# Performance work log

Hardware: AMD Instinct MI355X
Metric: run time of the kernel (lower is better)

The kernel has to match this reference:

```python
import jax, jax.numpy as jnp
import numpy as np

E = 512      # embed_size
H = 8        # heads
HD = E // H  # head_dim
TN = 288     # time_num
FE = 4       # forward_expansion
N, T = 64, 512


def layernorm(x, g, b, eps=1e-5):
    mu = jnp.mean(x, axis=-1, keepdims=True)
    var = jnp.mean((x - mu) ** 2, axis=-1, keepdims=True)
    return (x - mu) * jax.lax.rsqrt(var + eps) * g + b


def setup_inputs() -> dict:
    key = jax.random.key(0)
    ks = jax.random.split(key, 12)
    w = lambda k, sh: jax.random.normal(k, sh, dtype=jnp.float32) * 0.02
    return {
        "value": jax.random.normal(ks[0], (N, T, E), dtype=jnp.float32),
        "key_in": jax.random.normal(ks[1], (N, T, E), dtype=jnp.float32),
        "query": jax.random.normal(ks[2], (N, T, E), dtype=jnp.float32),
        "i": 37,
        # One_hot_encoder params: learned identity-init table + linear to embed
        "I_mat": jnp.eye(TN, dtype=jnp.float32),
        "oh_W": w(ks[3], (TN, E)), "oh_b": jnp.zeros((E,), jnp.float32),
        # per-head projections (shared across heads, as in the torch module)
        "Wv": w(ks[4], (HD, HD)), "Wk": w(ks[5], (HD, HD)), "Wq": w(ks[6], (HD, HD)),
        "Wo": w(ks[7], (E, E)), "bo": jnp.zeros((E,), jnp.float32),
        "g1": jnp.ones((E,), jnp.float32), "b1": jnp.zeros((E,), jnp.float32),
        "g2": jnp.ones((E,), jnp.float32), "b2": jnp.zeros((E,), jnp.float32),
        "W1": w(ks[8], (E, FE * E)), "bf1": jnp.zeros((FE * E,), jnp.float32),
        "W2": w(ks[9], (FE * E, E)), "bf2": jnp.zeros((E,), jnp.float32),
    }


def reference(value, key_in, query, i, I_mat, oh_W, oh_b, Wv, Wk, Wq, Wo, bo,
              g1, b1, g2, b2, W1, bf1, W2, bf2):
    n, t, c = query.shape
    # One_hot_encoder: rows i..i+T-1 (mod time_num) of learned table -> linear
    rows = (i + jnp.arange(t)) % TN
    onehot = I_mat[rows] @ oh_W + oh_b            # (T, E), broadcast over N
    q_in = query + onehot[None, :, :]
    # per-head projections
    v = value.reshape(n, t, H, HD) @ Wv           # (N,T,H,HD)
    k = key_in.reshape(n, t, H, HD) @ Wk
    qh = q_in.reshape(n, t, H, HD) @ Wq
    # attention (note: scale uses sqrt(embed_size), per original code)
    energy = jnp.einsum("nqhd,nkhd->nhqk", qh, k) / jnp.sqrt(jnp.float32(E))
    attn = jax.nn.softmax(energy, axis=-1)
    out = jnp.einsum("nhqk,nkhd->nqhd", attn, v).reshape(n, t, E)
    out = out @ Wo + bo
    # residual + LN + FFN + residual + LN (dropout=0 -> identity)
    x = layernorm(out + q_in, g1, b1)
    ff = jax.nn.relu(x @ W1 + bf1) @ W2 + bf2
    return layernorm(ff + x, g2, b2)
```

## Files before the change

kernel.cpp:

```cpp
#include <hip/hip_runtime.h>

typedef __attribute__((ext_vector_type(8))) short s16x8;
typedef __attribute__((ext_vector_type(4))) float f32x4;

#define TN 288

__device__ __forceinline__ unsigned short f2bf(float f) {
  union { float f; unsigned u; } v; v.f = f;
  unsigned r = v.u + 0x7fffu + ((v.u >> 16) & 1u);
  return (unsigned short)(r >> 16);
}
__device__ __forceinline__ float bf2f(unsigned short u) {
  union { float f; unsigned u; } v; v.u = ((unsigned)u) << 16;
  return v.f;
}
__device__ __forceinline__ unsigned lds_addr(const void* p) {
  return (unsigned)(unsigned long long)(const __attribute__((address_space(3))) char*)p;
}
__device__ __forceinline__ void async_copy16(unsigned short* lds, const unsigned short* g) {
  __builtin_amdgcn_global_load_lds(
      (const __attribute__((address_space(1))) unsigned int*)g,
      (__attribute__((address_space(3))) unsigned int*)lds, 16, 0, 0);
}

__device__ __forceinline__ void pack_body(const float* __restrict__ W,
    unsigned short* __restrict__ out, int N, long t) {
  int lr = (int)(t & 15);
  int lg = (int)((t >> 4) & 3);
  long g6 = t >> 6;
  int nt = N >> 4;
  int n16 = (int)(g6 % nt);
  int kb = (int)(g6 / nt) << 5;
  int k = kb + lg * 8;
  int col = n16 * 16 + lr;
  s16x8 v;
#pragma unroll
  for (int j = 0; j < 8; ++j) v[j] = (short)f2bf(W[(size_t)(k + j) * N + col]);
  *(s16x8*)(out + t * 8) = v;
}

__global__ __launch_bounds__(256) void prep_kernel(const int* __restrict__ pi,
    const float* __restrict__ I_mat, const float* __restrict__ ohW,
    const float* __restrict__ ohb, float* __restrict__ onehot,
    const float* __restrict__ Wv, const float* __restrict__ Wk,
    const float* __restrict__ Wq, unsigned short* __restrict__ Wv_b,
    unsigned short* __restrict__ Wk_b, unsigned short* __restrict__ Wq_b,
    const float* __restrict__ Wo, const float* __restrict__ W1,
    const float* __restrict__ W2, unsigned short* __restrict__ Wop,
    unsigned short* __restrict__ W1p, unsigned short* __restrict__ W2p) {
  int b = blockIdx.x, tid = threadIdx.x;
  if (b < 512) {
    int t = b;
    int r = (pi[0] + t) % TN;
    float acc0 = ohb[tid], acc1 = ohb[tid + 256];
    const float* Ir = I_mat + (size_t)r * TN;
    for (int j = 0; j < TN; ++j) {
      float iv = Ir[j];
      acc0 += iv * ohW[(size_t)j * 512 + tid];
      acc1 += iv * ohW[(size_t)j * 512 + tid + 256];
    }
    onehot[(size_t)t * 512 + tid] = acc0;
    onehot[(size_t)t * 512 + tid + 256] = acc1;
  } else if (b < 640) {
    pack_body(Wo, Wop, 512, (long)(b - 512) * 256 + tid);
  } else if (b < 1152) {
    pack_body(W1, W1p, 2048, (long)(b - 640) * 256 + tid);
  } else if (b < 1664) {
    pack_body(W2, W2p, 512, (long)(b - 1152) * 256 + tid);
  } else {
    int which = b - 1664;
    const float* src = which == 0 ? Wv : (which == 1 ? Wk : Wq);
    unsigned short* dst = which == 0 ? Wv_b : (which == 1 ? Wk_b : Wq_b);
    float sc = which == 2 ? 0.06375871424f : 1.f;
#pragma unroll
    for (int j = 0; j < 4; ++j) {
      int i = tid * 16 + j * 4;
      float4 f = *(const float4*)(src + i);
      unsigned lo = (unsigned)f2bf(f.x * sc) | ((unsigned)f2bf(f.y * sc) << 16);
      unsigned hi = (unsigned)f2bf(f.z * sc) | ((unsigned)f2bf(f.w * sc) << 16);
      *(uint2*)(dst + i) = make_uint2(lo, hi);
    }
  }
}

__global__ __launch_bounds__(256) void proj_all(
    const float* __restrict__ value, const float* __restrict__ key_in,
    const float* __restrict__ query, const unsigned short* __restrict__ Wv_b,
    const unsigned short* __restrict__ Wk_b, const unsigned short* __restrict__ Wq_b,
    const float* __restrict__ onehot, unsigned short* __restrict__ vP,
    unsigned short* __restrict__ k_p, unsigned short* __restrict__ q_p) {
  __shared__ unsigned short As[64][40];
  __shared__ unsigned short Bs[64][40];
  __shared__ unsigned short Cs[64][72];
  const int which = blockIdx.x >> 12;
  const int mb = blockIdx.x & 4095;
  const float* A = which == 0 ? value : (which == 1 ? key_in : query);
  const unsigned short* B = which == 0 ? Wv_b : (which == 1 ? Wk_b : Wq_b);
  unsigned short* C = which == 0 ? vP : (which == 1 ? k_p : q_p);
  const bool qin = (which == 2);
  const int m0 = mb * 64;
  const int tid = threadIdx.x, w = tid >> 6, l = tid & 63, lr = l & 15, lg = l >> 4;
  const int wr = (w >> 1) * 32, wc = (w & 1) * 32;
  const int aRow = (tid * 8) >> 5, aK = (tid * 8) & 31;
  const int bK = (tid * 8) >> 6, bCol = (tid * 8) & 63;
  f32x4 acc[2][2] = {};
  for (int kb = 0; kb < 64; kb += 32) {
    size_t fl = (size_t)(m0 + aRow) * 64 + kb + aK;
    float4 f0 = *(const float4*)(A + fl);
    float4 f1 = *(const float4*)(A + fl + 4);
    if (qin) {
      const float* oh = onehot + (fl & 262143);
      float4 o0 = *(const float4*)(oh);
      float4 o1 = *(const float4*)(oh + 4);
      f0.x += o0.x; f0.y += o0.y; f0.z += o0.z; f0.w += o0.w;
      f1.x += o1.x; f1.y += o1.y; f1.z += o1.z; f1.w += o1.w;
    }
    s16x8 av;
    av[0] = (short)f2bf(f0.x); av[1] = (short)f2bf(f0.y);
    av[2] = (short)f2bf(f0.z); av[3] = (short)f2bf(f0.w);
    av[4] = (short)f2bf(f1.x); av[5] = (short)f2bf(f1.y);
    av[6] = (short)f2bf(f1.z); av[7] = (short)f2bf(f1.w);
    *(s16x8*)&As[aRow][aK] = av;
    s16x8 bv = *(const s16x8*)(B + (size_t)(kb + bK) * 64 + bCol);
#pragma unroll
    for (int j = 0; j < 8; ++j) Bs[bCol + j][bK] = (unsigned short)bv[j];
    __syncthreads();
    s16x8 af0 = *(const s16x8*)&As[wr + lr][lg * 8];
    s16x8 af1 = *(const s16x8*)&As[wr + 16 + lr][lg * 8];
    s16x8 bf0 = *(const s16x8*)&Bs[wc + lr][lg * 8];
    s16x8 bf1 = *(const s16x8*)&Bs[wc + 16 + lr][lg * 8];
    acc[0][0] = __builtin_amdgcn_mfma_f32_16x16x32_bf16(af0, bf0, acc[0][0], 0, 0, 0);
    acc[0][1] = __builtin_amdgcn_mfma_f32_16x16x32_bf16(af0, bf1, acc[0][1], 0, 0, 0);
    acc[1][0] = __builtin_amdgcn_mfma_f32_16x16x32_bf16(af1, bf0, acc[1][0], 0, 0, 0);
    acc[1][1] = __builtin_amdgcn_mfma_f32_16x16x32_bf16(af1, bf1, acc[1][1], 0, 0, 0);
    __syncthreads();
  }
  if (which != 0) {
#pragma unroll
    for (int fi = 0; fi < 2; ++fi)
#pragma unroll
      for (int fj = 0; fj < 2; ++fj)
#pragma unroll
        for (int r = 0; r < 4; ++r) {
          int row = m0 + wr + fi * 16 + lg * 4 + r;
          int col = wc + fj * 16 + lr;
          C[(size_t)row * 64 + col] = f2bf(acc[fi][fj][r]);
        }
  } else {
#pragma unroll
    for (int fi = 0; fi < 2; ++fi)
#pragma unroll
      for (int fj = 0; fj < 2; ++fj)
#pragma unroll
        for (int r = 0; r < 4; ++r)
          Cs[wr + fi * 16 + lg * 4 + r][wc + fj * 16 + lr] = f2bf(acc[fi][fj][r]);
    __syncthreads();
    int nIdx = m0 >> 12, t0 = (m0 >> 3) & 511;
    int cc = t0 >> 7, ksv = (t0 >> 5) & 3, lgv = (t0 >> 3) & 3;
#pragma unroll
    for (int it = 0; it < 2; ++it) {
      int p = tid + it * 256;
      int hh = p >> 6, d = p & 63;
      s16x8 vv;
#pragma unroll
      for (int j = 0; j < 8; ++j) vv[j] = (short)Cs[j * 8 + hh][d];
      size_t dst = ((size_t)(nIdx * 8 + hh)) * 32768 +
                   (size_t)(((cc * 16 + ksv * 4 + (d >> 4)) * 64) + lgv * 16 + (d & 15)) * 8;
      *(s16x8*)(C + dst) = vv;
    }
  }
}

template<bool RELU, bool OUTBF, bool RES>
__global__ __launch_bounds__(256) void gemmF(
    const unsigned short* __restrict__ A, int lda,
    const unsigned short* __restrict__ Bp, int ldbp, int nOff,
    const float* __restrict__ bias, void* __restrict__ Cout,
    const unsigned short* __restrict__ resid, int ldc,
    int M, int K, int nby) {
  __shared__ unsigned short As[2][8192];
  const int tid = threadIdx.x, w = tid >> 6, l = tid & 63, lr = l & 15, lg = l >> 4;
  const int nwg = gridDim.x;
  const int bid = (blockIdx.x & 7) * (nwg >> 3) + (blockIdx.x >> 3);
  const int bx = bid / nby, by = bid % nby;
  const int m0 = bx * 128;
  const int wr = (w >> 1) * 64, wc = (w & 1) * 64;
  const int srow = tid >> 3, sc8 = tid & 7;
  const int gcol = (sc8 ^ (srow & 7)) * 8;
  const unsigned short* Ag = A + (size_t)(m0 + srow) * lda + gcol;
  const size_t ldaa = (size_t)32 * lda;
  const unsigned short* Bg = Bp +
      ((size_t)(nOff >> 4) + by * 8 + (wc >> 4)) * 512 + lg * 128 + lr * 8;
  const size_t bks = (size_t)ldbp * 512;

  f32x4 acc[4][4] = {};
  s16x8 b0[4], b1[4];

#pragma unroll
  for (int it = 0; it < 4; ++it)
    async_copy16(&As[0][(it * 256 + tid) * 8], Ag + it * ldaa);
#pragma unroll
  for (int fj = 0; fj < 4; ++fj) {
    b0[fj] = *(const s16x8*)(Bg + fj * 512);
    b1[fj] = *(const s16x8*)(Bg + bks + fj * 512);
  }
  __syncthreads();

  int buf = 0;
  for (int kb = 0; kb < K; kb += 64) {
    int kn = (kb + 64 < K) ? kb + 64 : 0;
#pragma unroll
    for (int it = 0; it < 4; ++it)
      async_copy16(&As[buf ^ 1][(it * 256 + tid) * 8], Ag + kn + it * ldaa);
    s16x8 b0n[4];
    {
      const unsigned short* p = Bg + ((size_t)(kn >> 5)) * bks;
#pragma unroll
      for (int fj = 0; fj < 4; ++fj) b0n[fj] = *(const s16x8*)(p + fj * 512);
    }
    {
      s16x8 af[4];
#pragma unroll
      for (int fi = 0; fi < 4; ++fi) {
        int row = wr + fi * 16 + lr;
        af[fi] = *(const s16x8*)&As[buf][row * 64 + ((lg ^ (row & 7)) * 8)];
      }
#pragma unroll
      for (int fi = 0; fi < 4; ++fi)
#pragma unroll
        for (int fj = 0; fj < 4; ++fj)
          acc[fi][fj] = __builtin_amdgcn_mfma_f32_16x16x32_bf16(af[fi], b0[fj], acc[fi][fj], 0, 0, 0);
    }
    s16x8 b1n[4];
    {
      const unsigned short* p = Bg + ((size_t)((kn + 32) >> 5)) * bks;
#pragma unroll
      for (int fj = 0; fj < 4; ++fj) b1n[fj] = *(const s16x8*)(p + fj * 512);
    }
    {
      s16x8 af[4];
#pragma unroll
      for (int fi = 0; fi < 4; ++fi) {
        int row = wr + fi * 16 + lr;
        af[fi] = *(const s16x8*)&As[buf][row * 64 + (((4 + lg) ^ (row & 7)) * 8)];
      }
#pragma unroll
      for (int fi = 0; fi < 4; ++fi)
#pragma unroll
        for (int fj = 0; fj < 4; ++fj)
          acc[fi][fj] = __builtin_amdgcn_mfma_f32_16x16x32_bf16(af[fi], b1[fj], acc[fi][fj], 0, 0, 0);
    }
    __syncthreads();
#pragma unroll
    for (int fj = 0; fj < 4; ++fj) { b0[fj] = b0n[fj]; b1[fj] = b1n[fj]; }
    buf ^= 1;
  }

#pragma unroll
  for (int fj = 0; fj < 4; ++fj) {
    int colL = by * 128 + wc + fj * 16 + lr;
    float bv = bias[nOff + colL];
#pragma unroll
    for (int fi = 0; fi < 4; ++fi)
#pragma unroll
      for (int r = 0; r < 4; ++r) {
        int row = m0 + wr + fi * 16 + lg * 4 + r;
        size_t ci = (size_t)row * ldc + colL;
        float v = acc[fi][fj][r] + bv;
        if (RES) v += bf2f(resid[ci]);
        if (RELU) v = fmaxf(v, 0.f);
        if (OUTBF) ((unsigned short*)Cout)[ci] = f2bf(v);
        else ((float*)Cout)[ci] = v;
      }
  }
}

__global__ __launch_bounds__(256, 2) void attn_kernel(
    const unsigned short* __restrict__ Qp, const unsigned short* __restrict__ Kp,
    const unsigned short* __restrict__ Vt, unsigned short* __restrict__ Out) {
  __shared__ unsigned short KS[128][72];
  __shared__ unsigned short P[4][16][132];
  const int bid = blockIdx.x;
  const int qq = bid >> 9, g = bid & 511, h = g & 7, n = g >> 3;
  const int tid = threadIdx.x, w = tid >> 6, l = tid & 63, lr = l & 15, lg = l >> 4;
  const int q0 = qq * 128;

  s16x8 qf[2][2];
#pragma unroll
  for (int rt = 0; rt < 2; ++rt) {
    const size_t qb = (((size_t)(n * 512 + q0 + w * 32 + rt * 16 + lr)) * 8 + h) * 64;
    qf[rt][0] = *(const s16x8*)(Qp + qb + lg * 8);
    qf[rt][1] = *(const s16x8*)(Qp + qb + 32 + lg * 8);
  }
  const unsigned short* Vfb = Vt + ((size_t)(n * 8 + h)) * 32768 + (size_t)l * 8;

  f32x4 oacc[2][4] = {};
  float m[2][4], lsum[2][4];
#pragma unroll
  for (int rt = 0; rt < 2; ++rt)
#pragma unroll
    for (int r = 0; r < 4; ++r) { m[rt][r] = -1e30f; lsum[rt][r] = 0.f; }
  s16x8 vreg[16];

#pragma unroll
  for (int it = 0; it < 4; ++it) {
    int idx = tid + it * 256;
    int rr = idx >> 3, dd = (idx & 7) * 8;
    *(s16x8*)&KS[rr][dd] =
        *(const s16x8*)(Kp + (((size_t)(n * 512 + rr)) * 8 + h) * 64 + dd);
  }
#pragma unroll
  for (int i = 0; i < 16; ++i)
    vreg[i] = *(const s16x8*)(Vfb + ((size_t)i << 9));
  __syncthreads();

  for (int c = 0; c < 4; ++c) {
    if (c) {
      __syncthreads();
#pragma unroll
      for (int it = 0; it < 4; ++it) {
        int idx = tid + it * 256;
        int rr = idx >> 3, dd = (idx & 7) * 8;
        *(s16x8*)&KS[rr][dd] =
            *(const s16x8*)(Kp + (((size_t)(n * 512 + c * 128 + rr)) * 8 + h) * 64 + dd);
      }
#pragma unroll
      for (int i = 0; i < 16; ++i)
        vreg[i] = *(const s16x8*)(Vfb + ((size_t)(c * 16 + i) << 9));
      __syncthreads();
    }
#pragma unroll
    for (int rt = 0; rt < 2; ++rt) {
      f32x4 sacc[8];
      __builtin_amdgcn_s_setprio(1);
#pragma unroll
      for (int f = 0; f < 8; ++f) {
        s16x8 b0 = *(const s16x8*)&KS[f * 16 + lr][lg * 8];
        s16x8 b1 = *(const s16x8*)&KS[f * 16 + lr][32 + lg * 8];
        f32x4 a = {};
        a = __builtin_amdgcn_mfma_f32_16x16x32_bf16(qf[rt][0], b0, a, 0, 0, 0);
        a = __builtin_amdgcn_mfma_f32_16x16x32_bf16(qf[rt][1], b1, a, 0, 0, 0);
        sacc[f] = a;
      }
      __builtin_amdgcn_s_setprio(0);

      float fs[4];
#pragma unroll
      for (int r = 0; r < 4; ++r) {
        float cm = sacc[0][r];
#pragma unroll
        for (int f = 1; f < 8; ++f) cm = fmaxf(cm, sacc[f][r]);
#pragma unroll
        for (int mk = 1; mk < 16; mk <<= 1) cm = fmaxf(cm, __shfl_xor(cm, mk));
        float mn = fmaxf(m[rt][r], cm);
        fs[r] = __builtin_amdgcn_exp2f(m[rt][r] - mn);
        m[rt][r] = mn;
        unsigned pa = lds_addr(&P[w][lg * 4 + r][lr]);
        float cs = 0.f;
#pragma unroll
        for (int f = 0; f < 8; ++f) {
          float p = __builtin_amdgcn_exp2f(sacc[f][r] - mn);
          asm volatile("ds_write_b16_d16_hi %0, %1 offset:%2"
                       :: "v"(pa), "v"(p), "i"(f * 32) : "memory");
          cs += p;
        }
#pragma unroll
        for (int mk = 1; mk < 16; mk <<= 1) cs += __shfl_xor(cs, mk);
        lsum[rt][r] = lsum[rt][r] * fs[r] + cs;
      }
#pragma unroll
      for (int fj = 0; fj < 4; ++fj)
#pragma unroll
        for (int r = 0; r < 4; ++r) oacc[rt][fj][r] *= fs[r];

      asm volatile("s_waitcnt lgkmcnt(0)" ::: "memory");
      __builtin_amdgcn_sched_barrier(0);
      __builtin_amdgcn_s_setprio(1);
#pragma unroll
      for (int ks = 0; ks < 4; ++ks) {
        s16x8 pa = *(const s16x8*)&P[w][lr][ks * 32 + lg * 8];
#pragma unroll
        for (int fj = 0; fj < 4; ++fj)
          oacc[rt][fj] = __builtin_amdgcn_mfma_f32_16x16x32_bf16(pa, vreg[ks * 4 + fj], oacc[rt][fj], 0, 0, 0);
      }
      __builtin_amdgcn_s_setprio(0);
    }
  }

#pragma unroll
  for (int rt = 0; rt < 2; ++rt)
#pragma unroll
    for (int fj = 0; fj < 4; ++fj)
#pragma unroll
      for (int r = 0; r < 4; ++r) {
        int qrow = q0 + w * 32 + rt * 16 + lg * 4 + r;
        Out[((size_t)(n * 512 + qrow)) * 512 + h * 64 + fj * 16 + lr] =
            f2bf(oacc[rt][fj][r] / lsum[rt][r]);
      }
}

template<bool XBF, bool RES, bool RBF, bool QIN, bool OUTBF>
__global__ __launch_bounds__(256) void ln_kernel(const void* __restrict__ Xv,
    const void* __restrict__ Rv, const float* __restrict__ onehot,
    const float* __restrict__ g, const float* __restrict__ bb,
    void* __restrict__ outv) {
  int row = blockIdx.x * 4 + (threadIdx.x >> 6);
  int l = threadIdx.x & 63;
  size_t base = (size_t)row * 512 + l * 8;
  float v[8];
  if (XBF) {
    s16x8 xv = *(const s16x8*)((const unsigned short*)Xv + base);
#pragma unroll
    for (int j = 0; j < 8; ++j) v[j] = bf2f((unsigned short)xv[j]);
  } else {
    const float* X = (const float*)Xv;
    float4 x0 = *(const float4*)(X + base);
    float4 x1 = *(const float4*)(X + base + 4);
    v[0] = x0.x; v[1] = x0.y; v[2] = x0.z; v[3] = x0.w;
    v[4] = x1.x; v[5] = x1.y; v[6] = x1.z; v[7] = x1.w;
  }
  if (RES) {
    if (RBF) {
      s16x8 rv = *(const s16x8*)((const unsigned short*)Rv + base);
#pragma unroll
      for (int j = 0; j < 8; ++j) v[j] += bf2f((unsigned short)rv[j]);
    } else {
      const float* R = (const float*)Rv;
      float4 r0 = *(const float4*)(R + base);
      float4 r1 = *(const float4*)(R + base + 4);
      v[0] += r0.x; v[1] += r0.y; v[2] += r0.z; v[3] += r0.w;
      v[4] += r1.x; v[5] += r1.y; v[6] += r1.z; v[7] += r1.w;
    }
  }
  if (QIN) {
    size_t ob = (size_t)(row & 511) * 512 + l * 8;
    float4 o0 = *(const float4*)(onehot + ob);
    float4 o1 = *(const float4*)(onehot + ob + 4);
    v[0] += o0.x; v[1] += o0.y; v[2] += o0.z; v[3] += o0.w;
    v[4] += o1.x; v[5] += o1.y; v[6] += o1.z; v[7] += o1.w;
  }
  float s = 0.f, ss = 0.f;
#pragma unroll
  for (int j = 0; j < 8; ++j) { s += v[j]; ss += v[j] * v[j]; }
#pragma unroll
  for (int mk = 1; mk < 64; mk <<= 1) { s += __shfl_xor(s, mk); ss += __shfl_xor(ss, mk); }
  float mu = s * (1.f / 512.f);
  float inv = rsqrtf(ss * (1.f / 512.f) - mu * mu + 1e-5f);
#pragma unroll
  for (int j = 0; j < 8; ++j) {
    int e = l * 8 + j;
    float y = (v[j] - mu) * inv * g[e] + bb[e];
    if (OUTBF) ((unsigned short*)outv)[base + j] = f2bf(y);
    else ((float*)outv)[base + j] = y;
  }
}

extern "C" void kernel_launch(void* const* d_in, const int* in_sizes, int n_in,
                              void* d_out, int out_size, void* d_ws, size_t ws_size,
                              hipStream_t stream) {
  const float* value  = (const float*)d_in[0];
  const float* key_in = (const float*)d_in[1];
  const float* query  = (const float*)d_in[2];
  const int*   pi     = (const int*)d_in[3];
  const float* I_mat  = (const float*)d_in[4];
  const float* ohW    = (const float*)d_in[5];
  const float* ohb    = (const float*)d_in[6];
  const float* Wv     = (const float*)d_in[7];
  const float* Wk     = (const float*)d_in[8];
  const float* Wq     = (const float*)d_in[9];
  const float* Wo     = (const float*)d_in[10];
  const float* bo     = (const float*)d_in[11];
  const float* g1     = (const float*)d_in[12];
  const float* b1     = (const float*)d_in[13];
  const float* g2     = (const float*)d_in[14];
  const float* b2     = (const float*)d_in[15];
  const float* W1     = (const float*)d_in[16];
  const float* bf1    = (const float*)d_in[17];
  const float* W2     = (const float*)d_in[18];
  const float* bf2    = (const float*)d_in[19];

  char* ws = (char*)d_ws;
  const size_t MB = 1024 * 1024;
  unsigned short* q_p  = (unsigned short*)d_out;
  unsigned short* k_p  = q_p + 16777216;
  unsigned short* vP     = (unsigned short*)(ws + 0);
  unsigned short* attn_o = (unsigned short*)(ws + 32 * MB);
  unsigned short* x_b    = (unsigned short*)(ws + 64 * MB);
  unsigned short* ff1h   = (unsigned short*)(ws + 0);
  float*          onehot = (float*)(ws + 96 * MB);
  unsigned short* Wv_b   = (unsigned short*)(ws + 97 * MB);
  unsigned short* Wk_b   = Wv_b + 4096;
  unsigned short* Wq_b   = Wk_b + 4096;
  unsigned short* Wop    = Wq_b + 4096;
  unsigned short* W1p    = Wop + 262144;
  unsigned short* W2p    = W1p + 1048576;

  prep_kernel<<<1667, 256, 0, stream>>>(pi, I_mat, ohW, ohb, onehot,
      Wv, Wk, Wq, Wv_b, Wk_b, Wq_b, Wo, W1, W2, Wop, W1p, W2p);

  proj_all<<<12288, 256, 0, stream>>>(value, key_in, query,
      Wv_b, Wk_b, Wq_b, onehot, vP, k_p, q_p);

  attn_kernel<<<2048, 256, 0, stream>>>(q_p, k_p, vP, attn_o);

  gemmF<false, true, false><<<1024, 256, 0, stream>>>(
      attn_o, 512, Wop, 32, 0, bo, x_b, nullptr, 512, 32768, 512, 4);
  ln_kernel<true, true, false, true, true><<<8192, 256, 0, stream>>>(
      x_b, query, onehot, g1, b1, x_b);

  for (int hf = 0; hf < 2; ++hf) {
    const unsigned short* xh = x_b + (size_t)hf * 16384 * 512;
    gemmF<true, true, false><<<2048, 256, 0, stream>>>(
        xh, 512, W1p, 128, 0, bf1, ff1h, nullptr, 2048, 16384, 512, 16);
    gemmF<false, false, true><<<512, 256, 0, stream>>>(
        ff1h, 2048, W2p, 32, 0, bf2, (float*)d_out + (size_t)hf * 16384 * 512,
        xh, 512, 16384, 2048, 4);
  }
  ln_kernel<false, false, false, false, false><<<8192, 256, 0, stream>>>(
      d_out, nullptr, nullptr, g2, b2, d_out);
}
```

Before: 438.5 us.

## Load K and V fragments directly from global memory in attention kernel

```diff
diff --git a/kernel.cpp b/kernel.cpp
--- a/kernel.cpp
+++ b/kernel.cpp
@@ -278,7 +278,6 @@
 __global__ __launch_bounds__(256, 2) void attn_kernel(
     const unsigned short* __restrict__ Qp, const unsigned short* __restrict__ Kp,
     const unsigned short* __restrict__ Vt, unsigned short* __restrict__ Out) {
-  __shared__ unsigned short KS[128][72];
   __shared__ unsigned short P[4][16][132];
   const int bid = blockIdx.x;
   const int qq = bid >> 9, g = bid & 511, h = g & 7, n = g >> 3;
@@ -293,6 +292,7 @@
     qf[rt][1] = *(const s16x8*)(Qp + qb + 32 + lg * 8);
   }
   const unsigned short* Vfb = Vt + ((size_t)(n * 8 + h)) * 32768 + (size_t)l * 8;
+  const unsigned short* Kb = Kp + ((size_t)(n * 512) << 9) + h * 64 + (size_t)lr * 512 + lg * 8;
 
   f32x4 oacc[2][4] = {};
   float m[2][4], lsum[2][4];
@@ -300,49 +300,33 @@
   for (int rt = 0; rt < 2; ++rt)
 #pragma unroll
     for (int r = 0; r < 4; ++r) { m[rt][r] = -1e30f; lsum[rt][r] = 0.f; }
-  s16x8 vreg[16];
-
-#pragma unroll
-  for (int it = 0; it < 4; ++it) {
-    int idx = tid + it * 256;
-    int rr = idx >> 3, dd = (idx & 7) * 8;
-    *(s16x8*)&KS[rr][dd] =
-        *(const s16x8*)(Kp + (((size_t)(n * 512 + rr)) * 8 + h) * 64 + dd);
-  }
-#pragma unroll
-  for (int i = 0; i < 16; ++i)
-    vreg[i] = *(const s16x8*)(Vfb + ((size_t)i << 9));
-  __syncthreads();
 
   for (int c = 0; c < 4; ++c) {
-    if (c) {
-      __syncthreads();
-#pragma unroll
-      for (int it = 0; it < 4; ++it) {
-        int idx = tid + it * 256;
-        int rr = idx >> 3, dd = (idx & 7) * 8;
-        *(s16x8*)&KS[rr][dd] =
-            *(const s16x8*)(Kp + (((size_t)(n * 512 + c * 128 + rr)) * 8 + h) * 64 + dd);
-      }
-#pragma unroll
-      for (int i = 0; i < 16; ++i)
-        vreg[i] = *(const s16x8*)(Vfb + ((size_t)(c * 16 + i) << 9));
-      __syncthreads();
-    }
 #pragma unroll
     for (int rt = 0; rt < 2; ++rt) {
+      const unsigned short* Kc = Kb + (size_t)(c * 128) * 512;
+      asm volatile("" : "+v"(Kc));
+      const unsigned short* Vc = Vfb + ((size_t)(c * 16) << 9);
+      asm volatile("" : "+v"(Vc));
+
       f32x4 sacc[8];
       __builtin_amdgcn_s_setprio(1);
 #pragma unroll
       for (int f = 0; f < 8; ++f) {
-        s16x8 b0 = *(const s16x8*)&KS[f * 16 + lr][lg * 8];
-        s16x8 b1 = *(const s16x8*)&KS[f * 16 + lr][32 + lg * 8];
+        const unsigned short* kr = Kc + (size_t)(f * 16) * 512;
+        s16x8 b0 = *(const s16x8*)(kr);
+        s16x8 b1 = *(const s16x8*)(kr + 32);
         f32x4 a = {};
         a = __builtin_amdgcn_mfma_f32_16x16x32_bf16(qf[rt][0], b0, a, 0, 0, 0);
         a = __builtin_amdgcn_mfma_f32_16x16x32_bf16(qf[rt][1], b1, a, 0, 0, 0);
         sacc[f] = a;
       }
       __builtin_amdgcn_s_setprio(0);
+
+      s16x8 vreg[16];
+#pragma unroll
+      for (int i = 0; i < 16; ++i)
+        vreg[i] = *(const s16x8*)(Vc + ((size_t)i << 9));
 
       float fs[4];
 #pragma unroll
```

Measured after the change: 494.6 us. 12.8% more time.
